# Optimization experiments

Hardware: AMD Instinct MI355X
Metric: run time of the kernel (lower is better)

Reference implementation:

```python
import jax, jax.numpy as jnp
import numpy as np

B, S, E, H = 2, 2048, 1024, 16
DH = E // H
SCALE = DH ** -0.5

def setup_inputs() -> dict:
    key = jax.random.key(0)
    ks = jax.random.split(key, 5)
    w_std = (2.0 / (E + E)) ** 0.5  # xavier-ish scale
    return {
        'x': jax.random.normal(ks[0], (B, S, E), jnp.float32),
        'Wq': jax.random.normal(ks[1], (E, E), jnp.float32) * w_std,
        'bq': jnp.zeros((E,), jnp.float32),
        'Wk': jax.random.normal(ks[2], (E, E), jnp.float32) * w_std,
        'bk': jnp.zeros((E,), jnp.float32),
        'Wv': jax.random.normal(ks[3], (E, E), jnp.float32) * w_std,
        'bv': jnp.zeros((E,), jnp.float32),
        'Wo': jax.random.normal(ks[4], (E, E), jnp.float32) * w_std,
        'bo': jnp.zeros((E,), jnp.float32),
    }

def reference(x, Wq, bq, Wk, bk, Wv, bv, Wo, bo):
    # self-attention: query = key = value = x; torch Linear: y = x @ W.T + b
    q = (x @ Wq.T + bq) * SCALE            # [B,S,E]
    k = x @ Wk.T + bk
    v = x @ Wv.T + bv
    # split heads -> [B,S,H,DH]
    q = q.reshape(B, S, H, DH)
    k = k.reshape(B, S, H, DH)
    v = v.reshape(B, S, H, DH)
    # explicit attention matrix [B,H,S,S] (faithful to unfused bmm path)
    scores = jnp.einsum('bqhd,bkhd->bhqk', q, k)
    probs = jax.nn.softmax(scores, axis=-1)
    attn = jnp.einsum('bhqk,bkhd->bqhd', probs, v).reshape(B, S, E)
    return attn @ Wo.T + bo                # [B,S,E]
```

## Files before the change

kernel.cpp:

```cpp
#include <hip/hip_runtime.h>
#include <stdint.h>

#define BB 2
#define SS 2048
#define EE 1024
#define HH 16
#define DHD 64
#define MM (BB*SS)
#define QSCALE (0.125f * 1.4426950408889634f)

typedef __bf16 bf16;
typedef __bf16 bf16x8 __attribute__((ext_vector_type(8)));
typedef __bf16 bf16x4 __attribute__((ext_vector_type(4)));
typedef __bf16 bf16x2 __attribute__((ext_vector_type(2)));
typedef float  f32x4  __attribute__((ext_vector_type(4)));
typedef float  f32x16 __attribute__((ext_vector_type(16)));
typedef unsigned short ushort8 __attribute__((ext_vector_type(8)));

#define MFMA16(a,b,c) __builtin_amdgcn_mfma_f32_16x16x32_bf16(a,b,c,0,0,0)
#define MFMA32(a,b,c) __builtin_amdgcn_mfma_f32_32x32x16_bf16(a,b,c,0,0,0)

__device__ __forceinline__ void gload_lds16(const void* g, void* l) {
  __builtin_amdgcn_global_load_lds(
      (const __attribute__((address_space(1))) unsigned int*)g,
      (__attribute__((address_space(3))) unsigned int*)l, 16, 0, 0);
}

__device__ __forceinline__ unsigned short f2bf(float f) {
  union { float f; unsigned u; } v; v.f = f;
  return (unsigned short)((v.u + 0x7FFFu + ((v.u >> 16) & 1u)) >> 16);
}

__global__ void convert_kernel(const float* __restrict__ x,
                               const float* __restrict__ wq, const float* __restrict__ wk,
                               const float* __restrict__ wv, const float* __restrict__ wo,
                               unsigned short* __restrict__ xbf,
                               unsigned short* __restrict__ wqb, unsigned short* __restrict__ wkb,
                               unsigned short* __restrict__ wvb, unsigned short* __restrict__ wob) {
  long t = (long)blockIdx.x * blockDim.x + threadIdx.x;
  long base = t * 8;
  const float* src; unsigned short* dst; long off;
  if (base < 4194304L) { src = x; dst = xbf; off = base; }
  else {
    long r = base - 4194304L; int j = (int)(r >> 20); off = r & 1048575L;
    src = (j==0)?wq:(j==1)?wk:(j==2)?wv:wo;
    dst = (j==0)?wqb:(j==1)?wkb:(j==2)?wvb:wob;
  }
  const float4* s4 = (const float4*)(src + off);
  float4 a = s4[0], b = s4[1];
  ushort8 o;
  o[0]=f2bf(a.x); o[1]=f2bf(a.y); o[2]=f2bf(a.z); o[3]=f2bf(a.w);
  o[4]=f2bf(b.x); o[5]=f2bf(b.y); o[6]=f2bf(b.z); o[7]=f2bf(b.w);
  *(ushort8*)(dst + off) = o;
}

#define GS_STAGE(kbuf, kt) { \
    const size_t kb_ = (size_t)(kt) * 64; \
    char* d_ = lds + (kbuf) * 16384 + tid * 16; \
    gload_lds16(a0 + kb_, d_); \
    gload_lds16(a1 + kb_, d_ + 4096); \
    gload_lds16(b0 + kb_, d_ + 8192); \
    gload_lds16(b1 + kb_, d_ + 12288); \
  }

template<bool SWAP>
__device__ __forceinline__ void gemm_kloop(
    const char* a0, const char* a1, const char* b0, const char* b1,
    char* lds, const int tid, const int (&aoff)[4], const int (&boff)[4],
    f32x4 (&acc)[4][4]) {
  GS_STAGE(0, 0);
  GS_STAGE(1, 1);
  int cur = 0;
  for (int kt = 0; kt < 32; ++kt) {
    if (kt < 31) {
      asm volatile("s_waitcnt vmcnt(4)" ::: "memory");
    } else {
      asm volatile("s_waitcnt vmcnt(0)" ::: "memory");
    }
    __builtin_amdgcn_s_barrier();
    if (kt < 30) {
      int sb = cur + 2; if (sb >= 3) sb -= 3;
      GS_STAGE(sb, kt + 2);
    }
    const char* Ts = lds + cur * 16384;
    bf16x8 af[4], bfv[4];
#pragma unroll
    for (int mt=0; mt<4; ++mt) af[mt] = *(const bf16x8*)(Ts + aoff[mt]);
#pragma unroll
    for (int nt=0; nt<4; ++nt) bfv[nt] = *(const bf16x8*)(Ts + boff[nt]);
#pragma unroll
    for (int mt=0; mt<4; ++mt)
#pragma unroll
      for (int nt=0; nt<4; ++nt)
        acc[mt][nt] = SWAP ? MFMA16(bfv[nt], af[mt], acc[mt][nt])
                           : MFMA16(af[mt], bfv[nt], acc[mt][nt]);
    cur = (cur == 2) ? 0 : cur + 1;
  }
}

__global__ __launch_bounds__(256) void qkv_gemm(
    const bf16* __restrict__ xbf,
    const bf16* __restrict__ wqb, const bf16* __restrict__ wkb, const bf16* __restrict__ wvb,
    const float* __restrict__ bq, const float* __restrict__ bk, const float* __restrict__ bv,
    bf16* __restrict__ Q, bf16* __restrict__ K, bf16* __restrict__ VT) {
  __shared__ char lds[49152] __attribute__((aligned(16)));
  const int tid = threadIdx.x;
  const int bm = blockIdx.y * 128;
  const int bnG = blockIdx.x * 128;
  const int proj = bnG >> 10;
  const int bn = bnG & 1023;
  const bf16* wsel = (proj==0)?wqb:(proj==1)?wkb:wvb;
  const float* bias = (proj==0)?bq:(proj==1)?bk:bv;

  const int lane = tid & 63, w = tid >> 6;
  const int wm = (w>>1)*64, wn = (w&1)*64;
  const int c = lane & 15, g = lane >> 4;

  const int sr = tid >> 2;
  const int scb = ((tid & 3) * 16) ^ ((sr & 3) << 4);
  const char* a0 = (const char*)xbf  + ((size_t)(bm + sr     ) * 1024) * 2 + scb;
  const char* a1 = (const char*)xbf  + ((size_t)(bm + 64 + sr) * 1024) * 2 + scb;
  const char* b0 = (const char*)wsel + ((size_t)(bn + sr     ) * 1024) * 2 + scb;
  const char* b1 = (const char*)wsel + ((size_t)(bn + 64 + sr) * 1024) * 2 + scb;

  int aoff[4], boff[4];
#pragma unroll
  for (int mt=0; mt<4; ++mt) { int rr = wm + mt*16 + c; aoff[mt] = rr*64 + ((g*16) ^ ((rr&3)<<4)); }
#pragma unroll
  for (int nt=0; nt<4; ++nt) { int rr = wn + nt*16 + c; boff[nt] = 8192 + rr*64 + ((g*16) ^ ((rr&3)<<4)); }

  f32x4 acc[4][4];
#pragma unroll
  for (int mt=0; mt<4; ++mt)
#pragma unroll
    for (int nt=0; nt<4; ++nt) acc[mt][nt] = (f32x4){0.f,0.f,0.f,0.f};

  const int bidx = bm >> 11;
  const int srow = bm & 2047;

  if (proj != 2) {
    gemm_kloop<true>(a0, a1, b0, b1, lds, tid, aoff, boff, acc);
    bf16* dst = (proj == 0) ? Q : K;
    const float qs = (proj == 0) ? QSCALE : 1.0f;
#pragma unroll
    for (int nt=0; nt<4; ++nt) {
      const int n0 = bn + wn + nt*16 + g*4;
      const float4 b4 = *(const float4*)(bias + n0);
      const int h = n0 >> 6, d0 = n0 & 63;
#pragma unroll
      for (int mt=0; mt<4; ++mt) {
        const int s = srow + wm + mt*16 + c;
        bf16x4 pk;
        pk[0] = (bf16)((acc[mt][nt][0] + b4.x) * qs);
        pk[1] = (bf16)((acc[mt][nt][1] + b4.y) * qs);
        pk[2] = (bf16)((acc[mt][nt][2] + b4.z) * qs);
        pk[3] = (bf16)((acc[mt][nt][3] + b4.w) * qs);
        *(bf16x4*)(dst + (((size_t)(bidx*16 + h))*2048 + s)*64 + d0) = pk;
      }
    }
  } else {
    gemm_kloop<false>(a0, a1, b0, b1, lds, tid, aoff, boff, acc);
#pragma unroll
    for (int nt=0; nt<4; ++nt) {
      const int n = bn + wn + nt*16 + c;
      const float bv_ = bias[n];
      const int h = n >> 6, d = n & 63;
#pragma unroll
      for (int mt=0; mt<4; ++mt) {
        const int m0 = wm + mt*16 + g*4;
        bf16x4 pk;
#pragma unroll
        for (int r=0;r<4;++r) pk[r] = (bf16)(acc[mt][nt][r] + bv_);
        *(bf16x4*)(VT + (((size_t)(bidx*16 + h))*64 + d)*2048 + (srow + m0)) = pk;
      }
    }
  }
}

__global__ __launch_bounds__(512) void attn_kernel(
    const bf16* __restrict__ Q, const bf16* __restrict__ K,
    const bf16* __restrict__ VT, bf16* __restrict__ attn_out) {
  __shared__ char alds[32768] __attribute__((aligned(16)));
  const int tid = threadIdx.x;
  const int L = tid & 63, wid = tid >> 6;
  const int q5 = L & 31, h = L >> 5;
  const int bh = blockIdx.y;
  const int qbase = blockIdx.x * 256;
  const bf16* Qh = Q + (size_t)bh * 2048 * 64;
  const char* Khb = (const char*)(K  + (size_t)bh * 2048 * 64);
  const char* Vhb = (const char*)(VT + (size_t)bh * 64 * 2048);

  const int srow = tid >> 3, sch = tid & 7;
  const int ssw = ((sch ^ (srow & 7)) << 4);
  const char* srcK = Khb + (size_t)srow * 128  + ssw;
  const char* srcV = Vhb + (size_t)srow * 4096 + ssw;

#define ATT_STAGE(buf, kv) { \
    gload_lds16(srcK + (size_t)(kv) * 128, alds + (buf) * 16384 + tid * 16); \
    gload_lds16(srcV + (size_t)(kv) * 2,   alds + (buf) * 16384 + 8192 + tid * 16); \
  }

  const int qrow = qbase + wid * 32 + q5;
  bf16x8 qf[4];
#pragma unroll
  for (int dk = 0; dk < 4; ++dk)
    qf[dk] = *(const bf16x8*)(Qh + (size_t)qrow * 64 + dk * 16 + h * 8);

  f32x16 o0 = {0,0,0,0,0,0,0,0,0,0,0,0,0,0,0,0};
  f32x16 o1 = {0,0,0,0,0,0,0,0,0,0,0,0,0,0,0,0};
  float m = -1e30f, l = 0.f;

  ATT_STAGE(0, 0);
  asm volatile("s_waitcnt vmcnt(0)" ::: "memory");
  __builtin_amdgcn_s_barrier();

  for (int t = 0; t < 32; ++t) {
    const int cur = t & 1;
    if (t < 31) ATT_STAGE(cur ^ 1, (t + 1) * 64);

    const char* Kl = alds + cur * 16384;
    const char* Vl = Kl + 8192;

    f32x16 st0 = {0,0,0,0,0,0,0,0,0,0,0,0,0,0,0,0};
    f32x16 st1 = {0,0,0,0,0,0,0,0,0,0,0,0,0,0,0,0};
#pragma unroll
    for (int dk = 0; dk < 4; ++dk) {
      const int r0 = q5;
      bf16x8 k0 = *(const bf16x8*)(Kl + r0*128        + (((2*dk + h) ^ (r0 & 7)) << 4));
      const int r1 = 32 + q5;
      bf16x8 k1 = *(const bf16x8*)(Kl + r1*128        + (((2*dk + h) ^ (r1 & 7)) << 4));
      st0 = MFMA32(k0, qf[dk], st0);
      st1 = MFMA32(k1, qf[dk], st1);
    }

    float tmax = -1e30f;
#pragma unroll
    for (int r = 0; r < 16; ++r) { tmax = fmaxf(tmax, st0[r]); tmax = fmaxf(tmax, st1[r]); }
    tmax = fmaxf(tmax, __shfl_xor(tmax, 32, 64));
    if (!__all(tmax <= m + 8.f)) {
      const float mnew = fmaxf(m, tmax);
      const float corr = __builtin_exp2f(m - mnew);
      l *= corr;
      o0 *= corr; o1 *= corr;
      m = mnew;
    }

    unsigned pk0[4][2], pk1[4][2];
    float ps = 0.f;
#pragma unroll
    for (int j = 0; j < 4; ++j)
#pragma unroll
      for (int a = 0; a < 2; ++a) {
        {
          float x0 = __builtin_exp2f(st0[4*j+2*a]     - m);
          float x1 = __builtin_exp2f(st0[4*j+2*a + 1] - m);
          ps += x0 + x1;
          union { bf16x2 v; unsigned u; } z; z.v[0] = (bf16)x0; z.v[1] = (bf16)x1;
          pk0[j][a] = z.u;
        }
        {
          float x0 = __builtin_exp2f(st1[4*j+2*a]     - m);
          float x1 = __builtin_exp2f(st1[4*j+2*a + 1] - m);
          ps += x0 + x1;
          union { bf16x2 v; unsigned u; } z; z.v[0] = (bf16)x0; z.v[1] = (bf16)x1;
          pk1[j][a] = z.u;
        }
      }
    ps += __shfl_xor(ps, 32, 64);
    l += ps;

    bf16x8 pf[4];
#pragma unroll
    for (int c = 0; c < 4; ++c) {
      const int cl = c & 1;
      unsigned own0, own1, snd0, snd1;
      if (c < 2) {
        own0 = h ? pk0[2*cl+1][0] : pk0[2*cl][0];
        own1 = h ? pk0[2*cl+1][1] : pk0[2*cl][1];
        snd0 = h ? pk0[2*cl][0]   : pk0[2*cl+1][0];
        snd1 = h ? pk0[2*cl][1]   : pk0[2*cl+1][1];
      } else {
        own0 = h ? pk1[2*cl+1][0] : pk1[2*cl][0];
        own1 = h ? pk1[2*cl+1][1] : pk1[2*cl][1];
        snd0 = h ? pk1[2*cl][0]   : pk1[2*cl+1][0];
        snd1 = h ? pk1[2*cl][1]   : pk1[2*cl+1][1];
      }
      unsigned sx0 = (unsigned)__shfl_xor((int)snd0, 32, 64);
      unsigned sx1 = (unsigned)__shfl_xor((int)snd1, 32, 64);
      union { unsigned u[4]; bf16x8 v; } fr;
      fr.u[0] = h ? sx0 : own0;
      fr.u[1] = h ? sx1 : own1;
      fr.u[2] = h ? own0 : sx0;
      fr.u[3] = h ? own1 : sx1;
      pf[c] = fr.v;
    }

#pragma unroll
    for (int c = 0; c < 4; ++c) {
      const int r0 = q5;
      bf16x8 v0 = *(const bf16x8*)(Vl + r0*128        + (((2*c + h) ^ (r0 & 7)) << 4));
      const int r1 = 32 + q5;
      bf16x8 v1 = *(const bf16x8*)(Vl + r1*128        + (((2*c + h) ^ (r1 & 7)) << 4));
      o0 = MFMA32(v0, pf[c], o0);
      o1 = MFMA32(v1, pf[c], o1);
    }

    if (t < 31) {
      asm volatile("s_waitcnt vmcnt(0)" ::: "memory");
      __builtin_amdgcn_s_barrier();
    }
  }
#undef ATT_STAGE

  const float inv = 1.0f / l;
  const int b = bh >> 4, hh = bh & 15;
  bf16* outrow = attn_out + ((size_t)(b*2048 + qrow))*1024 + hh*64;
#pragma unroll
  for (int j = 0; j < 4; ++j) {
    bf16x4 ov;
#pragma unroll
    for (int i = 0; i < 4; ++i) ov[i] = (bf16)(o0[4*j+i] * inv);
    *(bf16x4*)(outrow + 8*j + 4*h) = ov;
#pragma unroll
    for (int i = 0; i < 4; ++i) ov[i] = (bf16)(o1[4*j+i] * inv);
    *(bf16x4*)(outrow + 32 + 8*j + 4*h) = ov;
  }
}

__global__ __launch_bounds__(256) void out_gemm(
    const bf16* __restrict__ A, const bf16* __restrict__ W,
    const float* __restrict__ bias, float* __restrict__ out) {
  __shared__ char lds[36864] __attribute__((aligned(16)));
  const int tid = threadIdx.x;
  const int bm = blockIdx.y * 64, bn = blockIdx.x * 128;
  const int lane = tid & 63, w = tid >> 6;
  const int c = lane & 15, g = lane >> 4;

  const int sr = tid >> 2;
  const int scb = ((tid & 3) * 16) ^ ((sr & 3) << 4);
  const char* a0 = (const char*)A + ((size_t)(bm + sr     ) * 1024) * 2 + scb;
  const char* b0 = (const char*)W + ((size_t)(bn + sr     ) * 1024) * 2 + scb;
  const char* b1 = (const char*)W + ((size_t)(bn + 64 + sr) * 1024) * 2 + scb;

#define OUT_STAGE(kbuf, kt) { \
    const size_t kb_ = (size_t)(kt) * 64; \
    char* d_ = lds + (kbuf) * 12288 + tid * 16; \
    gload_lds16(a0 + kb_, d_); \
    gload_lds16(b0 + kb_, d_ + 4096); \
    gload_lds16(b1 + kb_, d_ + 8192); \
  }

  int aoff[4], boff[2];
#pragma unroll
  for (int mt=0; mt<4; ++mt) { int rr = mt*16 + c; aoff[mt] = rr*64 + ((g*16) ^ ((rr&3)<<4)); }
#pragma unroll
  for (int nt=0; nt<2; ++nt) { int rr = w*32 + nt*16 + c; boff[nt] = 4096 + rr*64 + ((g*16) ^ ((rr&3)<<4)); }

  f32x4 acc[4][2];
#pragma unroll
  for (int mt=0; mt<4; ++mt)
#pragma unroll
    for (int nt=0; nt<2; ++nt) acc[mt][nt] = (f32x4){0.f,0.f,0.f,0.f};

  OUT_STAGE(0, 0);
  OUT_STAGE(1, 1);
  int cur = 0;
  for (int kt = 0; kt < 32; ++kt) {
    if (kt < 31) {
      asm volatile("s_waitcnt vmcnt(3)" ::: "memory");
    } else {
      asm volatile("s_waitcnt vmcnt(0)" ::: "memory");
    }
    __builtin_amdgcn_s_barrier();
    if (kt < 30) {
      int sb = cur + 2; if (sb >= 3) sb -= 3;
      OUT_STAGE(sb, kt + 2);
    }
    const char* Ts = lds + cur * 12288;
    bf16x8 af[4], bfv[2];
#pragma unroll
    for (int mt=0; mt<4; ++mt) af[mt] = *(const bf16x8*)(Ts + aoff[mt]);
#pragma unroll
    for (int nt=0; nt<2; ++nt) bfv[nt] = *(const bf16x8*)(Ts + boff[nt]);
#pragma unroll
    for (int mt=0; mt<4; ++mt)
#pragma unroll
      for (int nt=0; nt<2; ++nt)
        acc[mt][nt] = MFMA16(bfv[nt], af[mt], acc[mt][nt]);
    cur = (cur == 2) ? 0 : cur + 1;
  }
#undef OUT_STAGE

#pragma unroll
  for (int nt=0; nt<2; ++nt) {
    const int n0 = bn + w*32 + nt*16 + g*4;
    const float4 b4 = *(const float4*)(bias + n0);
#pragma unroll
    for (int mt=0; mt<4; ++mt) {
      const int m0 = bm + mt*16 + c;
      float4 ov;
      ov.x = acc[mt][nt][0] + b4.x;
      ov.y = acc[mt][nt][1] + b4.y;
      ov.z = acc[mt][nt][2] + b4.z;
      ov.w = acc[mt][nt][3] + b4.w;
      *(float4*)(out + (size_t)m0*1024 + n0) = ov;
    }
  }
}

extern "C" void kernel_launch(void* const* d_in, const int* in_sizes, int n_in,
                              void* d_out, int out_size, void* d_ws, size_t ws_size,
                              hipStream_t stream) {
  const float* x  = (const float*)d_in[0];
  const float* Wq = (const float*)d_in[1];
  const float* bq = (const float*)d_in[2];
  const float* Wk = (const float*)d_in[3];
  const float* bk = (const float*)d_in[4];
  const float* Wv = (const float*)d_in[5];
  const float* bv = (const float*)d_in[6];
  const float* Wo = (const float*)d_in[7];
  const float* bo = (const float*)d_in[8];

  char* ws = (char*)d_ws;
  const size_t MiB = 1u << 20;
  unsigned short* xbf = (unsigned short*)(ws);
  unsigned short* wqb = (unsigned short*)(ws +  8*MiB);
  unsigned short* wkb = (unsigned short*)(ws + 10*MiB);
  unsigned short* wvb = (unsigned short*)(ws + 12*MiB);
  unsigned short* wob = (unsigned short*)(ws + 14*MiB);
  bf16* Qb    = (bf16*)(ws + 16*MiB);
  bf16* Kb    = (bf16*)(ws + 24*MiB);
  bf16* VTb   = (bf16*)(ws + 32*MiB);
  bf16* attnb = (bf16*)(ws + 40*MiB);

  convert_kernel<<<4096, 256, 0, stream>>>(x, Wq, Wk, Wv, Wo, xbf, wqb, wkb, wvb, wob);
  qkv_gemm<<<dim3(24, 32), 256, 0, stream>>>(
      (const bf16*)xbf, (const bf16*)wqb, (const bf16*)wkb, (const bf16*)wvb,
      bq, bk, bv, Qb, Kb, VTb);
  attn_kernel<<<dim3(8, 32), 512, 0, stream>>>(Qb, Kb, VTb, attnb);
  out_gemm<<<dim3(8, 64), 256, 0, stream>>>(attnb, (const bf16*)wob, bo, (float*)d_out);
}
```

Baseline: 203.4 us.

## Remap block indices for XCD-local L2 reuse and shrink attention blocks

Switches the three launches to 1D grids and remaps block IDs so blocks on the same XCD (bid&7) share rows of A or the same attention head, which should improve L2 hit rates on the chiplet design. The attention kernel also drops from 512 to 256 threads per block, with 128 query rows per block and 512 blocks, so each thread now issues two K and two V LDS loads per stage. This gives more blocks in flight and better head locality, but halves the number of query rows that reuse each staged K/V tile.

```diff
diff --git a/kernel.cpp b/kernel.cpp
--- a/kernel.cpp
+++ b/kernel.cpp
@@ -105,8 +105,13 @@
     bf16* __restrict__ Q, bf16* __restrict__ K, bf16* __restrict__ VT) {
   __shared__ char lds[49152] __attribute__((aligned(16)));
   const int tid = threadIdx.x;
-  const int bm = blockIdx.y * 128;
-  const int bnG = blockIdx.x * 128;
+  const int bid = blockIdx.x;
+  const int xcd = bid & 7;
+  const int ii = bid >> 3;
+  const int col = ii >> 2;
+  const int row = xcd * 4 + (ii & 3);
+  const int bm = row * 128;
+  const int bnG = col * 128;
   const int proj = bnG >> 10;
   const int bn = bnG & 1023;
   const bf16* wsel = (proj==0)?wqb:(proj==1)?wkb:wvb;
@@ -177,15 +182,18 @@
   }
 }
 
-__global__ __launch_bounds__(512) void attn_kernel(
+__global__ __launch_bounds__(256) void attn_kernel(
     const bf16* __restrict__ Q, const bf16* __restrict__ K,
     const bf16* __restrict__ VT, bf16* __restrict__ attn_out) {
   __shared__ char alds[32768] __attribute__((aligned(16)));
   const int tid = threadIdx.x;
+  const int bid = blockIdx.x;
+  const int xcd = bid & 7;
+  const int ii = bid >> 3;
+  const int bh = (ii >> 4) * 8 + xcd;
+  const int qbase = (ii & 15) * 128;
   const int L = tid & 63, wid = tid >> 6;
   const int q5 = L & 31, h = L >> 5;
-  const int bh = blockIdx.y;
-  const int qbase = blockIdx.x * 256;
   const bf16* Qh = Q + (size_t)bh * 2048 * 64;
   const char* Khb = (const char*)(K  + (size_t)bh * 2048 * 64);
   const char* Vhb = (const char*)(VT + (size_t)bh * 64 * 2048);
@@ -196,8 +204,13 @@
   const char* srcV = Vhb + (size_t)srow * 4096 + ssw;
 
 #define ATT_STAGE(buf, kv) { \
-    gload_lds16(srcK + (size_t)(kv) * 128, alds + (buf) * 16384 + tid * 16); \
-    gload_lds16(srcV + (size_t)(kv) * 2,   alds + (buf) * 16384 + 8192 + tid * 16); \
+    const char* sk_ = srcK + (size_t)(kv) * 128; \
+    const char* sv_ = srcV + (size_t)(kv) * 2; \
+    char* d_ = alds + (buf) * 16384 + tid * 16; \
+    gload_lds16(sk_,           d_); \
+    gload_lds16(sk_ + 32*128,  d_ + 4096); \
+    gload_lds16(sv_,           d_ + 8192); \
+    gload_lds16(sv_ + 32*4096, d_ + 12288); \
   }
 
   const int qrow = qbase + wid * 32 + q5;
@@ -226,9 +239,9 @@
 #pragma unroll
     for (int dk = 0; dk < 4; ++dk) {
       const int r0 = q5;
-      bf16x8 k0 = *(const bf16x8*)(Kl + r0*128        + (((2*dk + h) ^ (r0 & 7)) << 4));
+      bf16x8 k0 = *(const bf16x8*)(Kl + r0*128 + (((2*dk + h) ^ (r0 & 7)) << 4));
       const int r1 = 32 + q5;
-      bf16x8 k1 = *(const bf16x8*)(Kl + r1*128        + (((2*dk + h) ^ (r1 & 7)) << 4));
+      bf16x8 k1 = *(const bf16x8*)(Kl + r1*128 + (((2*dk + h) ^ (r1 & 7)) << 4));
       st0 = MFMA32(k0, qf[dk], st0);
       st1 = MFMA32(k1, qf[dk], st1);
     }
@@ -298,9 +311,9 @@
 #pragma unroll
     for (int c = 0; c < 4; ++c) {
       const int r0 = q5;
-      bf16x8 v0 = *(const bf16x8*)(Vl + r0*128        + (((2*c + h) ^ (r0 & 7)) << 4));
+      bf16x8 v0 = *(const bf16x8*)(Vl + r0*128 + (((2*c + h) ^ (r0 & 7)) << 4));
       const int r1 = 32 + q5;
-      bf16x8 v1 = *(const bf16x8*)(Vl + r1*128        + (((2*c + h) ^ (r1 & 7)) << 4));
+      bf16x8 v1 = *(const bf16x8*)(Vl + r1*128 + (((2*c + h) ^ (r1 & 7)) << 4));
       o0 = MFMA32(v0, pf[c], o0);
       o1 = MFMA32(v1, pf[c], o1);
     }
@@ -332,7 +345,12 @@
     const float* __restrict__ bias, float* __restrict__ out) {
   __shared__ char lds[36864] __attribute__((aligned(16)));
   const int tid = threadIdx.x;
-  const int bm = blockIdx.y * 64, bn = blockIdx.x * 128;
+  const int bid = blockIdx.x;
+  const int xcd = bid & 7;
+  const int ii = bid >> 3;
+  const int col = ii >> 3;
+  const int rowb = xcd * 8 + (ii & 7);
+  const int bm = rowb * 64, bn = col * 128;
   const int lane = tid & 63, w = tid >> 6;
   const int c = lane & 15, g = lane >> 4;
 
@@ -434,9 +452,9 @@
   bf16* attnb = (bf16*)(ws + 40*MiB);
 
   convert_kernel<<<4096, 256, 0, stream>>>(x, Wq, Wk, Wv, Wo, xbf, wqb, wkb, wvb, wob);
-  qkv_gemm<<<dim3(24, 32), 256, 0, stream>>>(
+  qkv_gemm<<<768, 256, 0, stream>>>(
       (const bf16*)xbf, (const bf16*)wqb, (const bf16*)wkb, (const bf16*)wvb,
       bq, bk, bv, Qb, Kb, VTb);
-  attn_kernel<<<dim3(8, 32), 512, 0, stream>>>(Qb, Kb, VTb, attnb);
-  out_gemm<<<dim3(8, 64), 256, 0, stream>>>(attnb, (const bf16*)wob, bo, (float*)d_out);
-}
+  attn_kernel<<<512, 256, 0, stream>>>(Qb, Kb, VTb, attnb);
+  out_gemm<<<512, 256, 0, stream>>>(attnb, (const bf16*)wob, bo, (float*)d_out);
+}
```

After: 206.1 us. No clear change (+1.3%).
